# Kernel tuning notes

Hardware: AMD Instinct MI355X
Metric: run time of the kernel (lower is better)

## Reference

```python
import jax, jax.numpy as jnp
import numpy as np
from jax import lax

IN_CHANNELS = 4
STEPS_IN_ITR = 3


def one_step_ltm(x, T):
    # x: [B, H, W]; T: [B, 10, H, W] (9 stencil weight planes + bias plane)
    B, H, W = x.shape
    xp = jnp.pad(x, ((0, 0), (1, 1), (1, 1)))
    out = T[:, 9]
    k = 0
    # original ordering: X0..X2 scan row-offset with col-offset 0, X3..X5 col 1, X6..X8 col 2
    for dj in range(3):
        for di in range(3):
            out = out + xp[:, di:di + H, dj:dj + W] * T[:, k]
            k += 1
    return out


def setup_inputs() -> dict:
    key = jax.random.key(0)
    k1, k2, k3 = jax.random.split(key, 3)
    B, Tt, C, H, W = 8, 16, 1, 512, 512
    x = jax.random.uniform(k1, (B, Tt, C, H, W), dtype=jnp.float32)
    # stand-in unet: 3x3 SAME conv, in_channels -> 10
    W_unet = jax.random.normal(k2, (10, IN_CHANNELS, 3, 3), dtype=jnp.float32) * 0.1
    b_unet = jax.random.normal(k3, (10,), dtype=jnp.float32) * 0.1
    return {"x": x, "W_unet": W_unet, "b_unet": b_unet}


def reference(x, W_unet, b_unet):
    B, Tt, C, H, W = x.shape
    x_in = x[:, -IN_CHANNELS:, 0]  # [B, in_channels, H, W]
    T = lax.conv_general_dilated(
        x_in, W_unet, window_strides=(1, 1), padding='SAME',
        dimension_numbers=('NCHW', 'OIHW', 'NCHW')) + b_unet[None, :, None, None]

    xt0 = one_step_ltm(x[:, -1, 0], T)  # stored at t=0 WITHOUT sigmoid (as in original)

    def body(xt, _):
        for _j in range(STEPS_IN_ITR):
            xt = one_step_ltm(xt, T)
            xt = jax.nn.sigmoid(one_step_ltm(xt, T))
        return xt, xt

    _, xs = lax.scan(body, xt0, None, length=Tt - 1)  # [Tt-1, B, H, W]
    seq = jnp.concatenate([xt0[None], xs], axis=0)     # [Tt, B, H, W]
    seq = jnp.transpose(seq, (1, 0, 2, 3))             # [B, Tt, H, W]
    xout = jnp.zeros((B, Tt, C, H, W), dtype=x.dtype).at[:, :, 0].set(seq)
    return xout
```

## Files before the change

### kernel.cpp

```cpp
#include <hip/hip_runtime.h>
#include <hip/hip_fp16.h>
#include <math.h>

#define Bd 8
#define Td 16
#define Hd 512
#define Wd 512
#define HWc (Hd * Wd)
#define NPIX (Bd * HWc)

#define CT  16
#define CR  18
#define CP  20
#define CTH2 256

#define WCR 128
#define WCC 64
#define WH  6
#define WTR 140
#define WTC 76
#define NPR 38
#define WP2 78
#define FTH 1024
#define PRPG 6
#define PNG 26

#define FMAMIX_LO(acc, wv, hv) \
    asm("v_fma_mix_f32 %0, %1, %2, %0 op_sel:[0,0,0] op_sel_hi:[0,1,0]" \
        : "+v"(acc) : "v"(wv), "v"(hv))
#define FMAMIX_HI(acc, wv, hv) \
    asm("v_fma_mix_f32 %0, %1, %2, %0 op_sel:[0,1,0] op_sel_hi:[0,1,0]" \
        : "+v"(acc) : "v"(wv), "v"(hv))

__device__ __forceinline__ float hi_half_f32(unsigned h) {
    __half2 hh = *(__half2*)&h;
    return __half2float(__high2half(hh));
}

__global__ __launch_bounds__(CTH2)
void conv_step0_kernel(const float* __restrict__ x,
                       const float* __restrict__ Wu,
                       const float* __restrict__ bu,
                       __half2* __restrict__ T,
                       float* __restrict__ out) {
    __shared__ float sX[4][CR][CP];

    int bx  = blockIdx.x;
    int b   = bx >> 10;
    int rem = bx & 1023;
    int by  = rem >> 5;
    int bc  = rem & 31;
    int i0  = by * CT;
    int j0  = bc * CT;

    const float* xb = x + ((size_t)b * Td + 12) * HWc;
    int tid = threadIdx.x;

    for (int idx = tid; idx < 4 * CR * CR; idx += CTH2) {
        int ch = idx / (CR * CR);
        int r2 = idx - ch * (CR * CR);
        int r  = r2 / CR;
        int c  = r2 - r * CR;
        int gi = i0 + r - 1, gj = j0 + c - 1;
        float v = 0.0f;
        if ((unsigned)gi < (unsigned)Hd && (unsigned)gj < (unsigned)Wd)
            v = xb[(size_t)ch * HWc + gi * Wd + gj];
        sX[ch][r][c] = v;
    }
    __syncthreads();

    int tx = tid & 15;
    int ty = tid >> 4;

    float xf[36];
    #pragma unroll
    for (int ch = 0; ch < 4; ++ch)
        #pragma unroll
        for (int kh = 0; kh < 3; ++kh)
            #pragma unroll
            for (int kw = 0; kw < 3; ++kw)
                xf[(ch * 3 + kh) * 3 + kw] = sX[ch][ty + kh][tx + kw];

    int gi = i0 + ty;
    int gj = j0 + tx;
    size_t pix = (size_t)gi * Wd + gj;
    __half2* Tb = T + (size_t)b * 5 * HWc;

    float o0 = 0.0f;
    float accPrev = 0.0f;
    #pragma unroll
    for (int o = 0; o < 10; ++o) {
        const float* wo = Wu + o * 36;
        float acc = bu[o];
        #pragma unroll
        for (int z = 0; z < 36; ++z)
            acc += xf[z] * wo[z];

        if (o < 9)
            o0 += xf[(3 * 3 + (o % 3)) * 3 + (o / 3)] * acc;
        else
            o0 += acc;

        if (o & 1) {
            __half2 h = __floats2half2_rn(accPrev, acc);
            *(unsigned*)(Tb + (size_t)(o >> 1) * HWc + pix) = *(unsigned*)&h;
        }
        accPrev = acc;
    }

    out[(size_t)b * Td * HWc + pix] = o0;
}

__global__ __launch_bounds__(FTH, 2)
void fused6_pair32_kernel(const float* __restrict__ xin,
                          const __half2* __restrict__ T,
                          float* __restrict__ xout) {
    __shared__ __align__(16) float sA[WTR * WP2];
    __shared__ __align__(16) float sB[WTR * WP2];

    int tile = blockIdx.x;
    int b  = tile >> 5;
    int tr = (tile >> 3) & 3;
    int tc = tile & 7;
    int ri = tr * WCR - WH;
    int rj = tc * WCC - WH;

    const float* xb = xin + (size_t)b * Td * HWc;
    const __half2* Tb = T + (size_t)b * 5 * HWc;
    float* ob = xout + (size_t)b * Td * HWc;
    int tid = threadIdx.x;

    for (int idx = tid; idx < WTR * NPR; idx += FTH) {
        int r = idx / NPR, u = idx - r * NPR;
        int gi = ri + r, gj0 = rj + 2 * u;
        float v0 = 0.0f, v1 = 0.0f;
        if ((unsigned)gi < (unsigned)Hd && (unsigned)gj0 < (unsigned)Wd) {
            float2 f = *(const float2*)(xb + gi * Wd + gj0);
            v0 = f.x; v1 = f.y;
        }
        float2 st; st.x = v0; st.y = v1;
        *(float2*)&sA[r * WP2 + 2 * u] = st;
    }
    for (int idx = tid; idx < 2 * WTC; idx += FTH) {
        int r = (idx < WTC) ? 0 : (WTR - 1);
        int c = (idx < WTC) ? idx : idx - WTC;
        sB[r * WP2 + c] = 0.0f;
    }
    for (int idx = tid; idx < 2 * WTR; idx += FTH) {
        int r = (idx < WTR) ? idx : idx - WTR;
        int c = (idx < WTR) ? 0 : (WTC - 1);
        sB[r * WP2 + c] = 0.0f;
    }

    int g = tid / NPR;
    int u = tid - g * NPR;
    bool active = (g < PNG);
    int rs = 1 + g * PRPG;
    int c0 = 2 * u;
    int gj0 = rj + c0;
    bool pairin = (unsigned)gj0 < (unsigned)Wd;
    int offL = (u == 0) ? 0 : (c0 - 1);
    int offR = (u == NPR - 1) ? (WTC - 1) : (c0 + 2);

    unsigned tA[PRPG][5], tB[PRPG][5];
    #pragma unroll
    for (int jj = 0; jj < PRPG; ++jj) {
        int r  = rs + jj;
        int gi = ri + r;
        bool ok = active && (r <= WTR - 2) && ((unsigned)gi < (unsigned)Hd) && pairin;
        #pragma unroll
        for (int q = 0; q < 5; ++q) {
            uint2 pk; pk.x = 0u; pk.y = 0u;
            if (ok) pk = *(const uint2*)(Tb + (size_t)q * HWc + gi * Wd + gj0);
            tA[jj][q] = pk.x;
            tB[jj][q] = pk.y;
        }
    }
    __syncthreads();

    float* cur = sA;
    float* nxt = sB;

    #pragma unroll
    for (int s = 1; s <= 6; ++s) {
        if (active) {
            int base = (rs - 1) * WP2;
            float  Lp = cur[base + offL];
            float2 Mp = *(const float2*)&cur[base + c0];
            float  Rp = cur[base + offR];
            base += WP2;
            float  Lc = cur[base + offL];
            float2 Mc = *(const float2*)&cur[base + c0];
            float  Rc = cur[base + offR];
            #pragma unroll
            for (int jj = 0; jj < PRPG; ++jj) {
                int r  = rs + jj;
                int rn = (r + 1 <= WTR - 1) ? (r + 1) : (WTR - 1);
                int bn = rn * WP2;
                float  Ln = cur[bn + offL];
                float2 Mn = *(const float2*)&cur[bn + c0];
                float  Rn = cur[bn + offR];

                float a0 = hi_half_f32(tA[jj][4]);
                FMAMIX_LO(a0, Lp,   tA[jj][0]);
                FMAMIX_HI(a0, Lc,   tA[jj][0]);
                FMAMIX_LO(a0, Ln,   tA[jj][1]);
                FMAMIX_HI(a0, Mp.x, tA[jj][1]);
                FMAMIX_LO(a0, Mc.x, tA[jj][2]);
                FMAMIX_HI(a0, Mn.x, tA[jj][2]);
                FMAMIX_LO(a0, Mp.y, tA[jj][3]);
                FMAMIX_HI(a0, Mc.y, tA[jj][3]);
                FMAMIX_LO(a0, Mn.y, tA[jj][4]);
                float a1 = hi_half_f32(tB[jj][4]);
                FMAMIX_LO(a1, Mp.x, tB[jj][0]);
                FMAMIX_HI(a1, Mc.x, tB[jj][0]);
                FMAMIX_LO(a1, Mn.x, tB[jj][1]);
                FMAMIX_HI(a1, Mp.y, tB[jj][1]);
                FMAMIX_LO(a1, Mc.y, tB[jj][2]);
                FMAMIX_HI(a1, Mn.y, tB[jj][2]);
                FMAMIX_LO(a1, Rp,   tB[jj][3]);
                FMAMIX_HI(a1, Rc,   tB[jj][3]);
                FMAMIX_LO(a1, Rn,   tB[jj][4]);

                if ((s & 1) == 0) {
                    a0 = 1.0f / (1.0f + __expf(-a0));
                    a1 = 1.0f / (1.0f + __expf(-a1));
                }

                int gi = ri + r;
                bool inimg = ((unsigned)gi < (unsigned)Hd) && pairin;
                float v0 = inimg ? a0 : 0.0f;
                float v1 = inimg ? a1 : 0.0f;

                if (s < 6) {
                    if (r <= WTR - 2) {
                        if (u >= 1 && u <= NPR - 2) {
                            float2 st; st.x = v0; st.y = v1;
                            *(float2*)&nxt[r * WP2 + c0] = st;
                        } else if (u == 0) {
                            nxt[r * WP2 + 1] = v1;
                        } else {
                            nxt[r * WP2 + WTC - 2] = v0;
                        }
                    }
                } else {
                    if (u >= WH / 2 && u <= (WTC - 2 - WH) / 2 &&
                        r >= WH && r <= WTR - 1 - WH) {
                        float2 st; st.x = v0; st.y = v1;
                        *(float2*)(ob + gi * Wd + gj0) = st;
                    }
                }

                Lp = Lc; Mp = Mc; Rp = Rc;
                Lc = Ln; Mc = Mn; Rc = Rn;
            }
        }
        if (s < 6) {
            __syncthreads();
            float* tmp = cur; cur = nxt; nxt = tmp;
        }
    }
}

extern "C" void kernel_launch(void* const* d_in, const int* in_sizes, int n_in,
                              void* d_out, int out_size, void* d_ws, size_t ws_size,
                              hipStream_t stream) {
    const float* x  = (const float*)d_in[0];
    const float* Wu = (const float*)d_in[1];
    const float* bu = (const float*)d_in[2];
    float* out = (float*)d_out;
    __half2* T = (__half2*)d_ws;

    conv_step0_kernel<<<8192, CTH2, 0, stream>>>(x, Wu, bu, T, out);

    for (int t = 1; t < Td; ++t)
        fused6_pair32_kernel<<<256, FTH, 0, stream>>>(out + (size_t)(t - 1) * HWc, T,
                                                      out + (size_t)t * HWc);
}
```

Measured before the change: 479.5 us.

## Fuse two timesteps per launch with fp16-packed shared tiles and wider halo

Adds a kernel that runs 12 stencil steps (two output timesteps) per launch on a 128x64 core tile with a 12-pixel halo. It keeps the state in shared memory as packed half2 and uses mixed-precision FMA directly on the packed operands. This halves the number of launches and cuts how often state and T are reloaded from global memory. The cost is more redundant halo compute and fp16 storage of intermediate state, which may lose accuracy. A runtime check on register spills picks between this kernel and the old per-timestep path.

```diff
diff --git a/kernel.cpp b/kernel.cpp
--- a/kernel.cpp
+++ b/kernel.cpp
@@ -25,6 +25,17 @@
 #define PRPG 6
 #define PNG 26
 
+#define DCR 128
+#define DCC 64
+#define DH  12
+#define DTR 152
+#define DTC 88
+#define DNP 44
+#define DLP 45
+#define DTH 1024
+#define DRPG 7
+#define DNG 23
+
 #define FMAMIX_LO(acc, wv, hv) \
     asm("v_fma_mix_f32 %0, %1, %2, %0 op_sel:[0,0,0] op_sel_hi:[0,1,0]" \
         : "+v"(acc) : "v"(wv), "v"(hv))
@@ -32,9 +43,26 @@
     asm("v_fma_mix_f32 %0, %1, %2, %0 op_sel:[0,1,0] op_sel_hi:[0,1,0]" \
         : "+v"(acc) : "v"(wv), "v"(hv))
 
+#define FMIX_LL(acc, xv, tv) \
+    asm("v_fma_mix_f32 %0, %1, %2, %0 op_sel:[0,0,0] op_sel_hi:[1,1,0]" \
+        : "+v"(acc) : "v"(xv), "v"(tv))
+#define FMIX_LH(acc, xv, tv) \
+    asm("v_fma_mix_f32 %0, %1, %2, %0 op_sel:[0,1,0] op_sel_hi:[1,1,0]" \
+        : "+v"(acc) : "v"(xv), "v"(tv))
+#define FMIX_HL(acc, xv, tv) \
+    asm("v_fma_mix_f32 %0, %1, %2, %0 op_sel:[1,0,0] op_sel_hi:[1,1,0]" \
+        : "+v"(acc) : "v"(xv), "v"(tv))
+#define FMIX_HH(acc, xv, tv) \
+    asm("v_fma_mix_f32 %0, %1, %2, %0 op_sel:[1,1,0] op_sel_hi:[1,1,0]" \
+        : "+v"(acc) : "v"(xv), "v"(tv))
+
 __device__ __forceinline__ float hi_half_f32(unsigned h) {
     __half2 hh = *(__half2*)&h;
     return __half2float(__high2half(hh));
+}
+__device__ __forceinline__ unsigned pack2(float a, float b) {
+    __half2 h = __floats2half2_rn(a, b);
+    return *(unsigned*)&h;
 }
 
 __global__ __launch_bounds__(CTH2)
@@ -109,6 +137,160 @@
     }
 
     out[(size_t)b * Td * HWc + pix] = o0;
+}
+
+__global__ __launch_bounds__(DTH, 2)
+void fused12_pk_kernel(const float* __restrict__ xin,
+                       const __half2* __restrict__ T,
+                       float* __restrict__ xmid,
+                       float* __restrict__ xout) {
+    __shared__ unsigned sA2[DTR * DLP];
+    __shared__ unsigned sB2[DTR * DLP];
+
+    int tile = blockIdx.x;
+    int b  = tile >> 5;
+    int tr = (tile >> 3) & 3;
+    int tc = tile & 7;
+    int ri = tr * DCR - DH;
+    int rj = tc * DCC - DH;
+
+    const float* xb = xin + (size_t)b * Td * HWc;
+    const __half2* Tb = T + (size_t)b * 5 * HWc;
+    float* obm = xmid + (size_t)b * Td * HWc;
+    float* obo = xout + (size_t)b * Td * HWc;
+    int tid = threadIdx.x;
+
+    for (int idx = tid; idx < DTR * DNP; idx += DTH) {
+        int r = idx / DNP, u = idx - r * DNP;
+        int gi = ri + r, gj0 = rj + 2 * u;
+        unsigned v = 0u;
+        if ((unsigned)gi < (unsigned)Hd && (unsigned)gj0 < (unsigned)Wd) {
+            float2 f = *(const float2*)(xb + gi * Wd + gj0);
+            v = pack2(f.x, f.y);
+        }
+        sA2[r * DLP + u] = v;
+    }
+    for (int idx = tid; idx < 2 * DNP; idx += DTH) {
+        int r = (idx < DNP) ? 0 : (DTR - 1);
+        int u = (idx < DNP) ? idx : idx - DNP;
+        sB2[r * DLP + u] = 0u;
+    }
+    for (int idx = tid; idx < 2 * DTR; idx += DTH) {
+        int r = (idx < DTR) ? idx : idx - DTR;
+        int u = (idx < DTR) ? 0 : (DNP - 1);
+        sB2[r * DLP + u] = 0u;
+    }
+
+    int g = tid / DNP;
+    int u = tid - g * DNP;
+    bool active = (g < DNG);
+    int rs = 1 + g * DRPG;
+    int gj0 = rj + 2 * u;
+    bool pairin = (unsigned)gj0 < (unsigned)Wd;
+    int uL = (u == 0) ? 0 : u - 1;
+    int uR = (u == DNP - 1) ? (DNP - 1) : u + 1;
+
+    unsigned tA[DRPG][5], tB[DRPG][5];
+    #pragma unroll
+    for (int jj = 0; jj < DRPG; ++jj) {
+        int r  = rs + jj;
+        int gi = ri + r;
+        bool ok = active && (r <= DTR - 2) && ((unsigned)gi < (unsigned)Hd) && pairin;
+        #pragma unroll
+        for (int q = 0; q < 5; ++q) {
+            uint2 pk; pk.x = 0u; pk.y = 0u;
+            if (ok) pk = *(const uint2*)(Tb + (size_t)q * HWc + gi * Wd + gj0);
+            tA[jj][q] = pk.x;
+            tB[jj][q] = pk.y;
+        }
+    }
+    __syncthreads();
+
+    unsigned* cur = sA2;
+    unsigned* nxt = sB2;
+
+    #pragma unroll
+    for (int s = 1; s <= 12; ++s) {
+        if (active) {
+            int base = (rs - 1) * DLP;
+            unsigned Ap = cur[base + uL], Bp = cur[base + u], Cp = cur[base + uR];
+            base += DLP;
+            unsigned Ac = cur[base + uL], Bc = cur[base + u], Cc = cur[base + uR];
+            #pragma unroll
+            for (int jj = 0; jj < DRPG; ++jj) {
+                int r  = rs + jj;
+                int rn = (r + 1 <= DTR - 1) ? (r + 1) : (DTR - 1);
+                int bn = rn * DLP;
+                unsigned An = cur[bn + uL], Bn = cur[bn + u], Cn = cur[bn + uR];
+
+                float a0 = hi_half_f32(tA[jj][4]);
+                FMIX_HL(a0, Ap, tA[jj][0]);
+                FMIX_HH(a0, Ac, tA[jj][0]);
+                FMIX_HL(a0, An, tA[jj][1]);
+                FMIX_LH(a0, Bp, tA[jj][1]);
+                FMIX_LL(a0, Bc, tA[jj][2]);
+                FMIX_LH(a0, Bn, tA[jj][2]);
+                FMIX_HL(a0, Bp, tA[jj][3]);
+                FMIX_HH(a0, Bc, tA[jj][3]);
+                FMIX_HL(a0, Bn, tA[jj][4]);
+                float a1 = hi_half_f32(tB[jj][4]);
+                FMIX_LL(a1, Bp, tB[jj][0]);
+                FMIX_LH(a1, Bc, tB[jj][0]);
+                FMIX_LL(a1, Bn, tB[jj][1]);
+                FMIX_HH(a1, Bp, tB[jj][1]);
+                FMIX_HL(a1, Bc, tB[jj][2]);
+                FMIX_HH(a1, Bn, tB[jj][2]);
+                FMIX_LL(a1, Cp, tB[jj][3]);
+                FMIX_LH(a1, Cc, tB[jj][3]);
+                FMIX_LL(a1, Cn, tB[jj][4]);
+
+                if ((s & 1) == 0) {
+                    a0 = 1.0f / (1.0f + __expf(-a0));
+                    a1 = 1.0f / (1.0f + __expf(-a1));
+                }
+
+                int gi = ri + r;
+                bool inimg = ((unsigned)gi < (unsigned)Hd) && pairin;
+                float v0 = inimg ? a0 : 0.0f;
+                float v1 = inimg ? a1 : 0.0f;
+
+                bool corepx = (u >= DH / 2) && (u <= (DTC - 2 - DH) / 2) &&
+                              (r >= DH) && (r <= DTR - 1 - DH);
+                if (s < 12) {
+                    if (r <= DTR - 2) {
+                        int cell = r * DLP + u;
+                        if (u >= 1 && u <= DNP - 2) {
+                            nxt[cell] = pack2(v0, v1);
+                        } else if (u == 0) {
+                            __half h1 = __float2half_rn(v1);
+                            ((unsigned short*)nxt)[cell * 2 + 1] =
+                                *(unsigned short*)&h1;
+                        } else {
+                            __half h0 = __float2half_rn(v0);
+                            ((unsigned short*)nxt)[cell * 2] =
+                                *(unsigned short*)&h0;
+                        }
+                    }
+                    if (s == 6 && corepx) {
+                        float2 st; st.x = v0; st.y = v1;
+                        *(float2*)(obm + gi * Wd + gj0) = st;
+                    }
+                } else {
+                    if (corepx) {
+                        float2 st; st.x = v0; st.y = v1;
+                        *(float2*)(obo + gi * Wd + gj0) = st;
+                    }
+                }
+
+                Ap = Ac; Bp = Bc; Cp = Cc;
+                Ac = An; Bc = Bn; Cc = Cn;
+            }
+        }
+        if (s < 12) {
+            __syncthreads();
+            unsigned* tmp = cur; cur = nxt; nxt = tmp;
+        }
+    }
 }
 
 __global__ __launch_bounds__(FTH, 2)
@@ -273,7 +455,20 @@
 
     conv_step0_kernel<<<8192, CTH2, 0, stream>>>(x, Wu, bu, T, out);
 
-    for (int t = 1; t < Td; ++t)
-        fused6_pair32_kernel<<<256, FTH, 0, stream>>>(out + (size_t)(t - 1) * HWc, T,
-                                                      out + (size_t)t * HWc);
-}
+    hipFuncAttributes attr;
+    hipError_t qe = hipFuncGetAttributes(&attr, (const void*)fused12_pk_kernel);
+    bool useDouble = (qe == hipSuccess) && (attr.localSizeBytes == 0);
+
+    if (useDouble) {
+        for (int t = 1; t + 1 < Td; t += 2)
+            fused12_pk_kernel<<<256, DTH, 0, stream>>>(
+                out + (size_t)(t - 1) * HWc, T,
+                out + (size_t)t * HWc, out + (size_t)(t + 1) * HWc);
+        fused6_pair32_kernel<<<256, FTH, 0, stream>>>(
+            out + (size_t)14 * HWc, T, out + (size_t)15 * HWc);
+    } else {
+        for (int t = 1; t < Td; ++t)
+            fused6_pair32_kernel<<<256, FTH, 0, stream>>>(
+                out + (size_t)(t - 1) * HWc, T, out + (size_t)t * HWc);
+    }
+}
```

New measurement: 481.6 us. About the same (+0.4%).
